# Performance work log

Measured on AMD Instinct MI355X. Metric: run time of the kernel, lower is better.

Reference implementation:

```python
import jax, jax.numpy as jnp
import numpy as np
from jax import lax

STRIDE = 1
PADDING = 1


def setup_inputs() -> dict:
    key = jax.random.key(0)
    kx, kw = jax.random.split(key)
    x = jax.random.normal(kx, (32, 64, 64, 64), dtype=jnp.float32)
    # weights are angles uniform on (-pi, pi)
    weight = jax.random.uniform(kw, (128, 64, 3, 3), dtype=jnp.float32,
                                minval=-jnp.pi, maxval=jnp.pi)
    return {"x": x, "weight": weight}


def _ring_conv2d(x, weight, stride, padding):
    # out[b,o,i,j] = sum_{c,kh,kw} cos(x_pad[b,c,i*s+kh,j*s+kw] - w[o,c,kh,kw])
    # cos(a-b) = cos a cos b + sin a sin b  ->  two standard convolutions.
    # Pad the raw angles with zeros first (a padded zero contributes cos(-w)).
    p = padding
    xp = jnp.pad(x, ((0, 0), (0, 0), (p, p), (p, p)))
    dn = ('NCHW', 'OIHW', 'NCHW')
    out = lax.conv_general_dilated(jnp.cos(xp), jnp.cos(weight),
                                   window_strides=(stride, stride),
                                   padding='VALID', dimension_numbers=dn)
    out = out + lax.conv_general_dilated(jnp.sin(xp), jnp.sin(weight),
                                         window_strides=(stride, stride),
                                         padding='VALID', dimension_numbers=dn)
    return out


def reference(x, weight):
    return _ring_conv2d(x, weight, STRIDE, PADDING)
```

## Files before the change

kernel.cpp:

```cpp
#include <hip/hip_runtime.h>
#include <hip/hip_bf16.h>


typedef _Float16 half8 __attribute__((ext_vector_type(8)));
typedef float f32x16 __attribute__((ext_vector_type(16)));

#define NB 32
#define NC 64
#define NH 64
#define NW 64
#define NO 128
#define PW 66
#define TROWS 10
#define TCOLS 34
#define TPX (TROWS * TCOLS)
#define NLD (TPX * 4)

union U16 { unsigned short u; _Float16 h; };
union HB { uint4 u4; half8 h; };

__device__ inline unsigned pack_cs(float ang) {
    float s, c;
    sincosf(ang, &s, &c);
    U16 uc, us; uc.h = (_Float16)c; us.h = (_Float16)s;
    return (unsigned)uc.u | ((unsigned)us.u << 16);
}

__device__ inline unsigned pack_cs_fast(float ang) {
    float s, c;
    __sincosf(ang, &s, &c);
    U16 uc, us; uc.h = (_Float16)c; us.h = (_Float16)s;
    return (unsigned)uc.u | ((unsigned)us.u << 16);
}

__global__ __launch_bounds__(256) void prep_all(const float* __restrict__ x,
                                                const float* __restrict__ w,
                                                uint4* __restrict__ xp,
                                                uint4* __restrict__ wqa) {
    __shared__ unsigned ls[64 * 65];
    const int blk = blockIdx.x;
    const int t = threadIdx.x;

    if (blk < NB * NH) {
        const int b = blk >> 6, row = blk & 63;
#pragma unroll
        for (int pass = 0; pass < 16; ++pass) {
            int c = pass * 4 + (t >> 6);
            int col = t & 63;
            float v = x[((size_t)(b * NC + c) * NH + row) * NW + col];
            ls[c * 65 + col] = pack_cs_fast(v);
        }
        __syncthreads();
        const int q = t & 3, col = t >> 2;
#pragma unroll
        for (int cg = 0; cg < 4; ++cg) {
            uint4 vv;
            vv.x = ls[(cg * 16 + 4 * q + 0) * 65 + col];
            vv.y = ls[(cg * 16 + 4 * q + 1) * 65 + col];
            vv.z = ls[(cg * 16 + 4 * q + 2) * 65 + col];
            vv.w = ls[(cg * 16 + 4 * q + 3) * 65 + col];
            xp[(size_t)(((b * 4 + cg) * PW + row + 1) * PW + col + 1) * 4 + q] = vv;
        }
    } else if (blk < NB * NH + 72) {
        int tt = (blk - NB * NH) * 256 + t;
        if (tt < 36 * 2 * 128 * 2) {
            int g2 = tt & 1, o = (tt >> 1) & 127, kk = (tt >> 8) & 1, chunk = tt >> 9;
            int cg = chunk / 9, kpos = chunk % 9, kh = kpos / 3, kw = kpos % 3;
            unsigned r[4];
#pragma unroll
            for (int m = 0; m < 4; ++m) {
                int c = cg * 16 + kk * 8 + g2 * 4 + m;
                float ang = w[((o * NC + c) * 3 + kh) * 3 + kw];
                r[m] = pack_cs(ang);
            }
            wqa[tt] = make_uint4(r[0], r[1], r[2], r[3]);
        }
    } else {
        const int bc = blk - NB * NH - 72;
        uint4* base = xp + (size_t)bc * PW * PW * 4;
        const uint4 v = make_uint4(0x3C00u, 0x3C00u, 0x3C00u, 0x3C00u);
        for (int idx = t; idx < 260 * 4; idx += 256) {
            int p = idx >> 2, q = idx & 3;
            int r, c;
            if (p < 66)       { r = 0;       c = p; }
            else if (p < 132) { r = 65;      c = p - 66; }
            else if (p < 196) { r = p - 131; c = 0; }
            else              { r = p - 195; c = 65; }
            base[(size_t)(r * PW + c) * 4 + q] = v;
        }
    }
}

#define GLOAD16(gptr, ldsptr)                                                   \
    __builtin_amdgcn_global_load_lds(                                           \
        (const __attribute__((address_space(1))) unsigned*)(gptr),              \
        (__attribute__((address_space(3))) unsigned*)(ldsptr), 16, 0, 0)

__global__ __launch_bounds__(256, 2) void ring_conv(const uint4* __restrict__ xp,
                                                    const uint4* __restrict__ wqa,
                                                    float* __restrict__ out) {
    __shared__ __align__(16) char xs[2][NLD * 16];

    const int d = blockIdx.x;
    const int blk = (d & 7) * 64 + (d >> 3);

    const int ch2 = blk & 1, rq = (blk >> 1) & 7, b = blk >> 4;
    const int row0 = rq * 8, col0 = ch2 * 32;

    const int t = threadIdx.x, lane = t & 63, wid = t >> 6;
    const int l31 = lane & 31, g2 = lane >> 5;
    const int op = wid & 1, rg = wid >> 1;
    const int rowbase = rg * 4;

    f32x16 acc[2][4] = {};

    int goff[6];
#pragma unroll
    for (int k = 0; k < 6; ++k) {
        int e = wid * 340 + k * 64 + lane;
        if (e > NLD - 1) e = NLD - 1;
        int q = e / TPX, p = e - q * TPX;
        int rr = p / TCOLS, cc = p - rr * TCOLS;
        goff[k] = ((row0 + rr) * PW + (col0 + cc)) * 4 + q;
    }
    const int ebase = wid * 340;
    const size_t img_stride = (size_t)PW * PW * 4;
    const uint4* img0 = xp + (size_t)(b * 4) * img_stride;

#define STAGE(bufi, cgi)                                                        \
    {   const uint4* img = img0 + (size_t)(cgi) * img_stride;                   \
        _Pragma("unroll")                                                       \
        for (int k = 0; k < 5; ++k)                                             \
            GLOAD16(img + goff[k], &xs[bufi][(ebase + k * 64) * 16]);           \
        if (lane < 20) GLOAD16(img + goff[5], &xs[bufi][(ebase + 320) * 16]);   \
    }

    const uint4* wbase = wqa + (op * 64 + l31) * 2 + g2;

    STAGE(0, 0)
    asm volatile("s_waitcnt vmcnt(0)" ::: "memory");
    __builtin_amdgcn_sched_barrier(0);
    __builtin_amdgcn_s_barrier();

#pragma unroll
    for (int cg = 0; cg < 4; ++cg) {
        const int cur = cg & 1;

        if (cg < 3) {
            STAGE(cur ^ 1, cg + 1)
            asm volatile("s_waitcnt vmcnt(6)" ::: "memory");
        } else {
            asm volatile("s_waitcnt vmcnt(0)" ::: "memory");
        }
        __builtin_amdgcn_sched_barrier(0);
        __builtin_amdgcn_s_barrier();

        const char* xbuf = xs[cur];
        const uint4* wa = wbase + (size_t)(cg * 18) * 256;

        HB Ar[4][2];
#pragma unroll
        for (int i = 0; i < 4; ++i) {
            Ar[i][0].u4 = wa[i * 256];
            Ar[i][1].u4 = wa[i * 256 + 64];
        }
        HB Bop[2][4];
#pragma unroll
        for (int r = 0; r < 4; ++r)
            Bop[0][r].u4 = *(const uint4*)(xbuf
                + ((size_t)(g2 * TPX + (rowbase + r) * TCOLS + l31)) * 16);

#pragma unroll
        for (int s = 0; s < 18; ++s) {
            const int cp = s & 1, np = cp ^ 1;
            if (s < 17) {
                const int s1 = s + 1, kp1 = s1 >> 1, kk1 = s1 & 1;
                const int kh1 = kp1 / 3, kw1 = kp1 % 3;
#pragma unroll
                for (int r = 0; r < 4; ++r)
                    Bop[np][r].u4 = *(const uint4*)(xbuf
                        + ((size_t)((2 * kk1 + g2) * TPX
                                    + (rowbase + r + kh1) * TCOLS + l31 + kw1)) * 16);
            }
            __builtin_amdgcn_s_setprio(1);
#pragma unroll
            for (int r = 0; r < 4; ++r)
#pragma unroll
                for (int f = 0; f < 2; ++f)
                    acc[f][r] = __builtin_amdgcn_mfma_f32_32x32x16_f16(
                        Ar[s & 3][f].h, Bop[cp][r].h, acc[f][r], 0, 0, 0);
            __builtin_amdgcn_s_setprio(0);
            if (s < 14) {
                Ar[s & 3][0].u4 = wa[(s + 4) * 256];
                Ar[s & 3][1].u4 = wa[(s + 4) * 256 + 64];
            }
        }

        __builtin_amdgcn_s_barrier();
    }

#pragma unroll
    for (int f = 0; f < 2; ++f)
#pragma unroll
        for (int r = 0; r < 4; ++r) {
            const int orow = row0 + rowbase + r;
#pragma unroll
            for (int reg = 0; reg < 16; ++reg) {
                int o = op * 64 + f * 32 + (reg & 3) + 8 * (reg >> 2) + 4 * g2;
                out[(((size_t)b * NO + o) * NH + orow) * NW + col0 + l31] = acc[f][r][reg];
            }
        }
}

extern "C" void kernel_launch(void* const* d_in, const int* in_sizes, int n_in,
                              void* d_out, int out_size, void* d_ws, size_t ws_size,
                              hipStream_t stream) {
    const float* x = (const float*)d_in[0];
    const float* w = (const float*)d_in[1];

    uint4* xpnt = (uint4*)d_ws;
    uint4* wqp = (uint4*)((char*)d_ws + (size_t)36 * 1024 * 1024);

    prep_all<<<NB * NH + 72 + 128, 256, 0, stream>>>(x, w, xpnt, wqp);
    ring_conv<<<512, 256, 0, stream>>>(xpnt, wqp, (float*)d_out);
}
```

Measured before the change: 58.64 us.

## Reorder conv taps by column and reuse B-operand rows across kernel heights

The inner loop over the 9 kernel positions now runs in column-major order (kw outer, kh inner). For each kw, 6 input rows are loaded into registers once and reused across the three kh shifts, instead of reloading 4 rows per position. Weight fragments are now prefetched into a two-stage buffer, and the first loads are issued before the LDS wait and barrier. This cuts LDS read traffic. The cost is more registers, and the loads may be less well overlapped with the MFMAs, since the next B operands are no longer double-buffered.

```diff
diff --git a/kernel.cpp b/kernel.cpp
--- a/kernel.cpp
+++ b/kernel.cpp
@@ -145,6 +145,18 @@
 #pragma unroll
     for (int cg = 0; cg < 4; ++cg) {
         const int cur = cg & 1;
+        const uint4* wa = wbase + (size_t)(cg * 18) * 256;
+
+        HB Ar[2][2][2];
+#pragma unroll
+        for (int p = 0; p < 2; ++p) {
+            const int kpos = (p % 3) * 3 + (p / 3);
+#pragma unroll
+            for (int kk = 0; kk < 2; ++kk) {
+                Ar[p][kk][0].u4 = wa[(2 * kpos + kk) * 256];
+                Ar[p][kk][1].u4 = wa[(2 * kpos + kk) * 256 + 64];
+            }
+        }
 
         if (cg < 3) {
             STAGE(cur ^ 1, cg + 1)
@@ -156,43 +168,45 @@
         __builtin_amdgcn_s_barrier();
 
         const char* xbuf = xs[cur];
-        const uint4* wa = wbase + (size_t)(cg * 18) * 256;
-
-        HB Ar[4][2];
-#pragma unroll
-        for (int i = 0; i < 4; ++i) {
-            Ar[i][0].u4 = wa[i * 256];
-            Ar[i][1].u4 = wa[i * 256 + 64];
-        }
-        HB Bop[2][4];
-#pragma unroll
-        for (int r = 0; r < 4; ++r)
-            Bop[0][r].u4 = *(const uint4*)(xbuf
-                + ((size_t)(g2 * TPX + (rowbase + r) * TCOLS + l31)) * 16);
-
-#pragma unroll
-        for (int s = 0; s < 18; ++s) {
-            const int cp = s & 1, np = cp ^ 1;
-            if (s < 17) {
-                const int s1 = s + 1, kp1 = s1 >> 1, kk1 = s1 & 1;
-                const int kh1 = kp1 / 3, kw1 = kp1 % 3;
+
+        HB Bw[6][2];
+#pragma unroll
+        for (int p = 0; p < 9; ++p) {
+            const int kw = p / 3, kh = p % 3;
+            if (kh == 0) {
+#pragma unroll
+                for (int j = 0; j < 4; ++j)
+#pragma unroll
+                    for (int kk = 0; kk < 2; ++kk)
+                        Bw[j][kk].u4 = *(const uint4*)(xbuf
+                            + (size_t)((2 * kk + g2) * TPX
+                                       + (rowbase + j) * TCOLS + l31 + kw) * 16);
+            } else {
+                const int j = kh + 3;
+#pragma unroll
+                for (int kk = 0; kk < 2; ++kk)
+                    Bw[j][kk].u4 = *(const uint4*)(xbuf
+                        + (size_t)((2 * kk + g2) * TPX
+                                   + (rowbase + j) * TCOLS + l31 + kw) * 16);
+            }
+            __builtin_amdgcn_s_setprio(1);
+#pragma unroll
+            for (int kk = 0; kk < 2; ++kk)
 #pragma unroll
                 for (int r = 0; r < 4; ++r)
-                    Bop[np][r].u4 = *(const uint4*)(xbuf
-                        + ((size_t)((2 * kk1 + g2) * TPX
-                                    + (rowbase + r + kh1) * TCOLS + l31 + kw1)) * 16);
-            }
-            __builtin_amdgcn_s_setprio(1);
-#pragma unroll
-            for (int r = 0; r < 4; ++r)
-#pragma unroll
-                for (int f = 0; f < 2; ++f)
-                    acc[f][r] = __builtin_amdgcn_mfma_f32_32x32x16_f16(
-                        Ar[s & 3][f].h, Bop[cp][r].h, acc[f][r], 0, 0, 0);
+#pragma unroll
+                    for (int f = 0; f < 2; ++f)
+                        acc[f][r] = __builtin_amdgcn_mfma_f32_32x32x16_f16(
+                            Ar[p & 1][kk][f].h, Bw[r + kh][kk].h, acc[f][r], 0, 0, 0);
             __builtin_amdgcn_s_setprio(0);
-            if (s < 14) {
-                Ar[s & 3][0].u4 = wa[(s + 4) * 256];
-                Ar[s & 3][1].u4 = wa[(s + 4) * 256 + 64];
+            if (p < 7) {
+                const int p2 = p + 2;
+                const int kpos2 = (p2 % 3) * 3 + (p2 / 3);
+#pragma unroll
+                for (int kk = 0; kk < 2; ++kk) {
+                    Ar[p & 1][kk][0].u4 = wa[(2 * kpos2 + kk) * 256];
+                    Ar[p & 1][kk][1].u4 = wa[(2 * kpos2 + kk) * 256 + 64];
+                }
             }
         }
 
```

Result: no change. 58.29 us (-0.6%).
